# Performance work log

Measured on AMD Instinct MI355X. Metric: run time of the kernel, lower is better.

## Reference

```python
import jax, jax.numpy as jnp
import numpy as np

B, T, C, H, W = 2, 8, 256, 24, 24
NH = 8
HC = C // NH          # 32 head channels
KT, KHW = 3, 9        # offset conv kernel
ST, SHW = 2, 8        # offset conv stride
EPS = 1e-5


def _p(key, shape):
    return jax.random.normal(key, shape, dtype=jnp.float32) * 0.05


def setup_inputs() -> dict:
    ks = jax.random.split(jax.random.key(0), 16)
    return {
        "x": jax.random.normal(ks[0], (B, T, C, H, W), dtype=jnp.float32),
        "w_in": _p(ks[1], (C, C)), "b_in": _p(ks[2], (C,)),
        "w_q": _p(ks[3], (C, C)), "b_q": _p(ks[4], (C,)),
        "w_off_dw": _p(ks[5], (HC, 1, KT, KHW, KHW)), "b_off_dw": _p(ks[6], (HC,)),
        "ln_g": jnp.ones((HC,), jnp.float32), "ln_b": jnp.zeros((HC,), jnp.float32),
        "w_off_proj": _p(ks[7], (3, HC)),
        "w_k": _p(ks[8], (C, C)), "b_k": _p(ks[9], (C,)),
        "w_v": _p(ks[10], (C, C)), "b_v": _p(ks[11], (C,)),
        "rpe_w1": _p(ks[12], (32, 3)), "rpe_b1": _p(ks[13], (32,)),
        "rpe_w2": _p(ks[14], (1, 32)),
    }


def _conv1x1(x, w, b):
    # x: (B,C,T,H,W), w: (Co,Ci) -> pointwise Conv3d
    return jnp.einsum('bcthw,oc->bothw', x, w) + b[None, :, None, None, None]


def _trilinear(img, gx, gy, gz):
    # torch F.grid_sample(mode='bilinear', align_corners=True) for 5D input.
    # img: (G,Ch,T,H,W); gx->W axis, gy->H axis, gz->T axis, coords in [-1,1], shape (G,S)
    G, Ch, Td, Hd, Wd = img.shape
    ix = (gx + 1.0) * 0.5 * (Wd - 1)
    iy = (gy + 1.0) * 0.5 * (Hd - 1)
    iz = (gz + 1.0) * 0.5 * (Td - 1)
    x0 = jnp.floor(ix); y0 = jnp.floor(iy); z0 = jnp.floor(iz)
    fx = ix - x0; fy = iy - y0; fz = iz - z0
    x0i = jnp.clip(x0.astype(jnp.int32), 0, Wd - 1); x1i = jnp.clip(x0i + 1, 0, Wd - 1)
    y0i = jnp.clip(y0.astype(jnp.int32), 0, Hd - 1); y1i = jnp.clip(y0i + 1, 0, Hd - 1)
    z0i = jnp.clip(z0.astype(jnp.int32), 0, Td - 1); z1i = jnp.clip(z0i + 1, 0, Td - 1)
    bidx = jnp.arange(G)[:, None]

    def g(zi, yi, xi):
        return img[bidx, :, zi, yi, xi]  # (G,S,Ch)

    wz0, wz1 = (1.0 - fz)[..., None], fz[..., None]
    wy0, wy1 = (1.0 - fy)[..., None], fy[..., None]
    wx0, wx1 = (1.0 - fx)[..., None], fx[..., None]
    return (g(z0i, y0i, x0i) * wz0 * wy0 * wx0 + g(z0i, y0i, x1i) * wz0 * wy0 * wx1 +
            g(z0i, y1i, x0i) * wz0 * wy1 * wx0 + g(z0i, y1i, x1i) * wz0 * wy1 * wx1 +
            g(z1i, y0i, x0i) * wz1 * wy0 * wx0 + g(z1i, y0i, x1i) * wz1 * wy0 * wx1 +
            g(z1i, y1i, x0i) * wz1 * wy1 * wx0 + g(z1i, y1i, x1i) * wz1 * wy1 * wx1)


def reference(x, w_in, b_in, w_q, b_q, w_off_dw, b_off_dw, ln_g, ln_b, w_off_proj,
              w_k, b_k, w_v, b_v, rpe_w1, rpe_b1, rpe_w2):
    scale = HC ** (-0.5)
    xc = _conv1x1(jnp.transpose(x, (0, 2, 1, 3, 4)), w_in, b_in)       # (B,C,T,H,W)
    q = _conv1x1(xc, w_q, b_q)
    q_off = q.reshape(B * NH, HC, T, H, W)
    # depthwise offset conv: kernel (3,9,9), stride (2,8,8), pad (1,4,4)
    off = jax.lax.conv_general_dilated(
        q_off, w_off_dw, (ST, SHW, SHW),
        ((KT // 2, KT // 2), (KHW // 2, KHW // 2), (KHW // 2, KHW // 2)),
        dimension_numbers=('NCDHW', 'OIDHW', 'NCDHW'), feature_group_count=HC)
    off = off + b_off_dw[None, :, None, None, None]
    Tk, Hk, Wk = off.shape[2], off.shape[3], off.shape[4]
    o = jnp.transpose(off, (0, 2, 3, 4, 1))                             # (G,Tk,Hk,Wk,HC)
    mu = o.mean(-1, keepdims=True)
    var = ((o - mu) ** 2).mean(-1, keepdims=True)
    o = (o - mu) / jnp.sqrt(var + EPS) * ln_g + ln_b
    o = jax.nn.gelu(o, approximate=False)
    offset = jnp.einsum('bthwc,pc->bthwp', o, w_off_proj)               # (G,Tk,Hk,Wk,3)
    # reference points (linspace(0.5, K-0.5, K) normalized by (K-1))
    rt = ((jnp.arange(Tk, dtype=jnp.float32) + 0.5) / (Tk - 1.0)) * 2.0 - 1.0
    ry = ((jnp.arange(Hk, dtype=jnp.float32) + 0.5) / (Hk - 1.0)) * 2.0 - 1.0
    rx = ((jnp.arange(Wk, dtype=jnp.float32) + 0.5) / (Wk - 1.0)) * 2.0 - 1.0
    ref = jnp.stack(jnp.meshgrid(rt, ry, rx, indexing='ij'), axis=-1)   # (Tk,Hk,Wk,3)
    pos = jnp.clip(offset + ref, -1.0, 1.0)                             # offset_range_factor < 0 path
    G = B * NH
    n = Tk * Hk * Wk
    m = T * H * W
    posf = pos.reshape(G, n, 3)                                         # (t, y, x)
    # torch passes grid = pos[..., (0,2,1)] -> grid (x_w, y_h, z_t) = (pos_t, pos_x, pos_y)
    xs = _trilinear(xc.reshape(G, HC, T, H, W), posf[..., 0], posf[..., 2], posf[..., 1])  # (G,n,HC)
    x_sampled = jnp.transpose(xs, (0, 2, 1)).reshape(B, C, Tk, Hk, Wk)
    k = _conv1x1(x_sampled, w_k, b_k).reshape(G, HC, n)
    v = _conv1x1(x_sampled, w_v, b_v).reshape(G, HC, n)
    qf = q.reshape(G, HC, m)
    attn = jnp.einsum('bcm,bcn->bmn', qf, k) * scale                    # (G,m,n)
    # log-CPB bias (source normalizes y by W-1 and x by H-1; faithful)
    qt = (jnp.arange(T, dtype=jnp.float32) / (T - 1.0)) * 2.0 - 1.0
    qy = (jnp.arange(H, dtype=jnp.float32) / (W - 1.0)) * 2.0 - 1.0
    qx = (jnp.arange(W, dtype=jnp.float32) / (H - 1.0)) * 2.0 - 1.0
    qg = jnp.stack(jnp.meshgrid(qt, qy, qx, indexing='ij'), axis=-1).reshape(m, 3)
    disp = (qg[None, :, None, :] - posf[:, None, :, :]) * 4.0           # (G,m,n,3)
    disp = jnp.sign(disp) * jnp.log2(jnp.abs(disp) + 1.0) / 3.0         # log2(8) = 3
    hbias = jax.nn.relu(jnp.einsum('gmnp,hp->gmnh', disp, rpe_w1) + rpe_b1)
    attn = attn + jnp.einsum('gmnh,oh->gmno', hbias, rpe_w2)[..., 0]
    attn = jax.nn.softmax(attn, axis=2)
    out = jnp.einsum('bmn,bcn->bcm', attn, v).reshape(B, C, T, H, W)
    return jnp.transpose(out, (0, 2, 1, 3, 4))                          # (B,T,C,H,W)
```

## Files before the change

kernel.cpp:

```cpp
#include <hip/hip_runtime.h>
#include <hip/hip_bf16.h>

typedef unsigned short ushortT;
typedef __attribute__((ext_vector_type(8))) short bf16x8;
typedef __attribute__((ext_vector_type(4))) float f32x4;

#define WS_XC   0
#define WS_QB   2359296
#define WS_POS  3538944
#define WS_K    3540736
#define WS_V    3559168
#define WS_WC   3577600
#define WS_B512 3675904

__device__ __forceinline__ float bf2f(ushortT u) {
  union { unsigned int i; float f; } c; c.i = ((unsigned int)u) << 16; return c.f;
}
__device__ __forceinline__ ushortT f2bf(float f) {
  union { float f; unsigned int i; } c; c.f = f;
  unsigned int lsb = (c.i >> 16) & 1;
  return (ushortT)((c.i + 0x7fff + lsb) >> 16);
}
__device__ __forceinline__ float ldg_f(const void* p, int i, int bf) {
  return bf ? bf2f(((const ushortT*)p)[i]) : ((const float*)p)[i];
}
__device__ __forceinline__ int detect_bf(const void* x) {
  const ushortT* u = (const ushortT*)x;
  int wild = 0;
#pragma unroll
  for (int i = 0; i < 32; i++) {
    int e = (u[i] >> 7) & 0xFF;
    wild += (e != 0 && (e < 90 || e > 160)) ? 1 : 0;
  }
  return wild <= 4;
}

__global__ __launch_bounds__(256) void k_wc(const void* x, const void* w_in, const void* b_in,
                                            const void* w_q, const void* b_q,
                                            float* wc, float* bias512) {
  int o = blockIdx.x, tid = threadIdx.x;
  int bf = detect_bf(x);
  __shared__ float wq_s[256];
  __shared__ float red[256];
  wq_s[tid] = ldg_f(w_q, o * 256 + tid, bf);
  __syncthreads();
  float s = 0.f;
#pragma unroll 8
  for (int j = 0; j < 256; j++) s += wq_s[j] * ldg_f(w_in, j * 256 + tid, bf);
  wc[o * 256 + tid] = s;
  red[tid] = wq_s[tid] * ldg_f(b_in, tid, bf);
  __syncthreads();
  for (int m = 128; m; m >>= 1) {
    if (tid < m) red[tid] += red[tid + m];
    __syncthreads();
  }
  if (tid == 0) bias512[256 + o] = red[0] + ldg_f(b_q, o, bf);
  if (o == 0) bias512[tid] = ldg_f(b_in, tid, bf);
}

__global__ __launch_bounds__(256) void k_gemm_mfma(const void* x, const void* w_in, const float* wc,
                                                   const float* bias512, float* xc, ushortT* qb) {
  const int bf = detect_bf(x);
  __shared__ ushortT Ah[2][64 * 40], Al[2][64 * 40];
  __shared__ ushortT Bh[2][64 * 40], Bl[2][64 * 40];
  int tid = threadIdx.x;
  int bid = blockIdx.x;
  int colT = bid / 144, rowT = bid % 144;
  int col0 = colT * 64;
  int row0 = rowT * 64;
  int bt = row0 / 576;
  int hw0 = row0 % 576;
  const int isW = (col0 < 256);
  const ushortT* xB = (const ushortT*)x;
  const float*   xF = (const float*)x;
  const ushortT* wB = (const ushortT*)w_in;
  const float*   wF = (const float*)w_in;
  int ar = tid & 63, aoct = tid >> 6;
  int bn = tid >> 2, bko = tid & 3;
  int w = tid >> 6, l = tid & 63;
  int wr = w >> 1, wcq = w & 1;
  int lr = l & 15, lk = l >> 4;
  f32x4 acc[2][2] = {};

  float va[8], vb[8];
  auto loadA = [&](int kt) {
    int kbase = (bt * 256 + kt * 32 + aoct * 8) * 576 + hw0 + ar;
#pragma unroll
    for (int j = 0; j < 8; j++)
      va[j] = bf ? bf2f(xB[kbase + j * 576]) : xF[kbase + j * 576];
  };
  auto loadB = [&](int kt) {
    if (isW) {
      if (bf) {
        const ushortT* pp = wB + (col0 + bn) * 256 + kt * 32 + bko * 8;
#pragma unroll
        for (int j = 0; j < 8; j++) vb[j] = bf2f(pp[j]);
      } else {
        const float* pp = wF + (col0 + bn) * 256 + kt * 32 + bko * 8;
        float4 f0 = *(const float4*)pp;
        float4 f1 = *(const float4*)(pp + 4);
        vb[0] = f0.x; vb[1] = f0.y; vb[2] = f0.z; vb[3] = f0.w;
        vb[4] = f1.x; vb[5] = f1.y; vb[6] = f1.z; vb[7] = f1.w;
      }
    } else {
      const float* pp = wc + (col0 - 256 + bn) * 256 + kt * 32 + bko * 8;
      float4 f0 = *(const float4*)pp;
      float4 f1 = *(const float4*)(pp + 4);
      vb[0] = f0.x; vb[1] = f0.y; vb[2] = f0.z; vb[3] = f0.w;
      vb[4] = f1.x; vb[5] = f1.y; vb[6] = f1.z; vb[7] = f1.w;
    }
  };
  auto writeAB = [&](int buf) {
    unsigned ua[8], ra[8];
#pragma unroll
    for (int j = 0; j < 8; j++) {
      ua[j] = __float_as_uint(va[j]);
      ra[j] = __float_as_uint(va[j] - __uint_as_float(ua[j] & 0xffff0000u));
    }
    int4 ph, pl;
    ph.x = (int)((ua[0] >> 16) | (ua[1] & 0xffff0000u));
    ph.y = (int)((ua[2] >> 16) | (ua[3] & 0xffff0000u));
    ph.z = (int)((ua[4] >> 16) | (ua[5] & 0xffff0000u));
    ph.w = (int)((ua[6] >> 16) | (ua[7] & 0xffff0000u));
    pl.x = (int)((ra[0] >> 16) | (ra[1] & 0xffff0000u));
    pl.y = (int)((ra[2] >> 16) | (ra[3] & 0xffff0000u));
    pl.z = (int)((ra[4] >> 16) | (ra[5] & 0xffff0000u));
    pl.w = (int)((ra[6] >> 16) | (ra[7] & 0xffff0000u));
    *(int4*)&Ah[buf][ar * 40 + aoct * 8] = ph;
    *(int4*)&Al[buf][ar * 40 + aoct * 8] = pl;
#pragma unroll
    for (int j = 0; j < 8; j++) {
      ua[j] = __float_as_uint(vb[j]);
      ra[j] = __float_as_uint(vb[j] - __uint_as_float(ua[j] & 0xffff0000u));
    }
    ph.x = (int)((ua[0] >> 16) | (ua[1] & 0xffff0000u));
    ph.y = (int)((ua[2] >> 16) | (ua[3] & 0xffff0000u));
    ph.z = (int)((ua[4] >> 16) | (ua[5] & 0xffff0000u));
    ph.w = (int)((ua[6] >> 16) | (ua[7] & 0xffff0000u));
    pl.x = (int)((ra[0] >> 16) | (ra[1] & 0xffff0000u));
    pl.y = (int)((ra[2] >> 16) | (ra[3] & 0xffff0000u));
    pl.z = (int)((ra[4] >> 16) | (ra[5] & 0xffff0000u));
    pl.w = (int)((ra[6] >> 16) | (ra[7] & 0xffff0000u));
    *(int4*)&Bh[buf][bn * 40 + bko * 8] = ph;
    *(int4*)&Bl[buf][bn * 40 + bko * 8] = pl;
  };

  loadA(0); loadB(0);
  writeAB(0);
  __syncthreads();
  for (int kt = 0; kt < 8; kt++) {
    int cur = kt & 1;
    if (kt < 7) { loadA(kt + 1); loadB(kt + 1); }
    bf16x8 a0h = *(const bf16x8*)&Ah[cur][(wr * 32 + 0 * 16 + lr) * 40 + lk * 8];
    bf16x8 a1h = *(const bf16x8*)&Ah[cur][(wr * 32 + 1 * 16 + lr) * 40 + lk * 8];
    bf16x8 a0l = *(const bf16x8*)&Al[cur][(wr * 32 + 0 * 16 + lr) * 40 + lk * 8];
    bf16x8 a1l = *(const bf16x8*)&Al[cur][(wr * 32 + 1 * 16 + lr) * 40 + lk * 8];
    bf16x8 b0h = *(const bf16x8*)&Bh[cur][(wcq * 32 + 0 * 16 + lr) * 40 + lk * 8];
    bf16x8 b1h = *(const bf16x8*)&Bh[cur][(wcq * 32 + 1 * 16 + lr) * 40 + lk * 8];
    bf16x8 b0l = *(const bf16x8*)&Bl[cur][(wcq * 32 + 0 * 16 + lr) * 40 + lk * 8];
    bf16x8 b1l = *(const bf16x8*)&Bl[cur][(wcq * 32 + 1 * 16 + lr) * 40 + lk * 8];
    acc[0][0] = __builtin_amdgcn_mfma_f32_16x16x32_bf16(a0h, b0h, acc[0][0], 0, 0, 0);
    acc[0][0] = __builtin_amdgcn_mfma_f32_16x16x32_bf16(a0h, b0l, acc[0][0], 0, 0, 0);
    acc[0][0] = __builtin_amdgcn_mfma_f32_16x16x32_bf16(a0l, b0h, acc[0][0], 0, 0, 0);
    acc[0][1] = __builtin_amdgcn_mfma_f32_16x16x32_bf16(a0h, b1h, acc[0][1], 0, 0, 0);
    acc[0][1] = __builtin_amdgcn_mfma_f32_16x16x32_bf16(a0h, b1l, acc[0][1], 0, 0, 0);
    acc[0][1] = __builtin_amdgcn_mfma_f32_16x16x32_bf16(a0l, b1h, acc[0][1], 0, 0, 0);
    acc[1][0] = __builtin_amdgcn_mfma_f32_16x16x32_bf16(a1h, b0h, acc[1][0], 0, 0, 0);
    acc[1][0] = __builtin_amdgcn_mfma_f32_16x16x32_bf16(a1h, b0l, acc[1][0], 0, 0, 0);
    acc[1][0] = __builtin_amdgcn_mfma_f32_16x16x32_bf16(a1l, b0h, acc[1][0], 0, 0, 0);
    acc[1][1] = __builtin_amdgcn_mfma_f32_16x16x32_bf16(a1h, b1h, acc[1][1], 0, 0, 0);
    acc[1][1] = __builtin_amdgcn_mfma_f32_16x16x32_bf16(a1h, b1l, acc[1][1], 0, 0, 0);
    acc[1][1] = __builtin_amdgcn_mfma_f32_16x16x32_bf16(a1l, b1h, acc[1][1], 0, 0, 0);
    if (kt < 7) writeAB(cur ^ 1);
    __syncthreads();
  }
#pragma unroll
  for (int m = 0; m < 2; m++) {
#pragma unroll
    for (int n = 0; n < 2; n++) {
#pragma unroll
      for (int i = 0; i < 4; i++) {
        int row = row0 + wr * 32 + m * 16 + lk * 4 + i;
        int col = col0 + wcq * 32 + n * 16 + lr;
        float v = acc[m][n][i] + bias512[col];
        if (isW) xc[row * 256 + col] = v;
        else     qb[row * 256 + (col - 256)] = f2bf(v);
      }
    }
  }
}

__global__ __launch_bounds__(256) void k_offsets(const void* x, const ushortT* qb, const void* w_dw,
                                                 const void* b_dw, const void* ln_g, const void* ln_b,
                                                 const void* w_proj, float* pos) {
  __shared__ float wdw[243 * 33];
  __shared__ float part[8][33];
  int bid = blockIdx.x;
  int g = bid / 36, nn = bid % 36;
  int b = g >> 3, nh = g & 7;
  int tk = nn / 9, hk = (nn / 3) % 3, wk = nn % 3;
  int tid = threadIdx.x;
  int ch = tid & 31, grp = tid >> 5;
  int bf = detect_bf(x);
  for (int i = tid; i < 7776; i += 256) {
    int c = i / 243, tap = i % 243;
    wdw[tap * 33 + c] = ldg_f(w_dw, i, bf);
  }
  __syncthreads();
  float sum = 0.f;
  for (int tap = grp; tap < 243; tap += 8) {
    int dt = tap / 81, rem = tap % 81, dh = rem / 9, dw = rem % 9;
    int t = tk * 2 - 1 + dt, h = hk * 8 - 4 + dh, w = wk * 8 - 4 + dw;
    if (t < 0 || t >= 8 || h < 0 || h >= 24 || w < 0 || w >= 24) continue;
    float qv = bf2f(qb[((b * 8 + t) * 576 + h * 24 + w) * 256 + nh * 32 + ch]);
    sum += qv * wdw[tap * 33 + ch];
  }
  part[grp][ch] = sum;
  __syncthreads();
  if (tid < 32) {
    float v = ldg_f(b_dw, ch, bf);
#pragma unroll
    for (int j = 0; j < 8; j++) v += part[j][ch];
    float s1 = v;
    for (int m = 16; m; m >>= 1) s1 += __shfl_xor(s1, m);
    float mu = s1 * (1.f / 32.f);
    float d = v - mu;
    float s2 = d * d;
    for (int m = 16; m; m >>= 1) s2 += __shfl_xor(s2, m);
    float o = d * rsqrtf(s2 * (1.f / 32.f) + 1e-5f) * ldg_f(ln_g, ch, bf) + ldg_f(ln_b, ch, bf);
    o = 0.5f * o * (1.f + erff(o * 0.70710678118654752f));
    float res[3];
#pragma unroll
    for (int p = 0; p < 3; p++) {
      float t3 = o * ldg_f(w_proj, p * 32 + ch, bf);
      for (int m = 16; m; m >>= 1) t3 += __shfl_xor(t3, m);
      res[p] = t3;
    }
    if (ch == 0) {
      float ref0 = ((tk + 0.5f) / 3.f) * 2.f - 1.f;
      float ref1 = ((hk + 0.5f) / 2.f) * 2.f - 1.f;
      float ref2 = ((wk + 0.5f) / 2.f) * 2.f - 1.f;
      pos[bid * 3 + 0] = fminf(1.f, fmaxf(-1.f, res[0] + ref0));
      pos[bid * 3 + 1] = fminf(1.f, fmaxf(-1.f, res[1] + ref1));
      pos[bid * 3 + 2] = fminf(1.f, fmaxf(-1.f, res[2] + ref2));
    }
  }
}

__global__ __launch_bounds__(256) void k_svkv(const void* x, const float* xc_rm, const float* pos,
                                              const void* w_k, const void* b_k,
                                              const void* w_v, const void* b_v,
                                              float* k_rm, float* v_rm) {
  int bx = blockIdx.x;
  int row = bx >> 2, quad = bx & 3;
  int sel = quad >> 1, colhalf = quad & 1;
  int b = row / 36, nn = row % 36;
  int tid = threadIdx.x;
  int bf = detect_bf(x);
  __shared__ float a[256];
  {
    int nh = tid >> 5;
    int g = b * 8 + nh;
    float p0 = pos[(g * 36 + nn) * 3 + 0];
    float p1 = pos[(g * 36 + nn) * 3 + 1];
    float p2 = pos[(g * 36 + nn) * 3 + 2];
    float ix = (p0 + 1.f) * 0.5f * 23.f;
    float iy = (p2 + 1.f) * 0.5f * 23.f;
    float iz = (p1 + 1.f) * 0.5f * 7.f;
    float x0f = floorf(ix), y0f = floorf(iy), z0f = floorf(iz);
    float fx = ix - x0f, fy = iy - y0f, fz = iz - z0f;
    int x0 = min(max((int)x0f, 0), 23), x1 = min(x0 + 1, 23);
    int y0 = min(max((int)y0f, 0), 23), y1 = min(y0 + 1, 23);
    int z0 = min(max((int)z0f, 0), 7),  z1 = min(z0 + 1, 7);
#define AT(z, y, x) xc_rm[(((b * 8 + (z)) * 576 + (y) * 24 + (x)) * 256 + tid)]
    a[tid] =
      AT(z0, y0, x0) * (1.f - fz) * (1.f - fy) * (1.f - fx) + AT(z0, y0, x1) * (1.f - fz) * (1.f - fy) * fx +
      AT(z0, y1, x0) * (1.f - fz) * fy * (1.f - fx)         + AT(z0, y1, x1) * (1.f - fz) * fy * fx +
      AT(z1, y0, x0) * fz * (1.f - fy) * (1.f - fx)         + AT(z1, y0, x1) * fz * (1.f - fy) * fx +
      AT(z1, y1, x0) * fz * fy * (1.f - fx)                 + AT(z1, y1, x1) * fz * fy * fx;
#undef AT
  }
  __syncthreads();
  const void* w = sel ? w_v : w_k;
  const void* bb = sel ? b_v : b_k;
  int col = colhalf * 128 + (tid >> 1);
  int half = tid & 1;
  int c0 = half * 128;
  float s = 0.f;
  if (bf) {
    const ushortT* wp = (const ushortT*)w + col * 256 + c0;
#pragma unroll 4
    for (int c = 0; c < 128; c += 8) {
      ushort4 k0 = *(const ushort4*)(wp + c), k1 = *(const ushort4*)(wp + c + 4);
      s += a[c0+c+0]*bf2f(k0.x) + a[c0+c+1]*bf2f(k0.y) + a[c0+c+2]*bf2f(k0.z) + a[c0+c+3]*bf2f(k0.w)
         + a[c0+c+4]*bf2f(k1.x) + a[c0+c+5]*bf2f(k1.y) + a[c0+c+6]*bf2f(k1.z) + a[c0+c+7]*bf2f(k1.w);
    }
  } else {
    const float* wp = (const float*)w + col * 256 + c0;
#pragma unroll 8
    for (int c = 0; c < 128; c += 4) {
      float4 k4 = *(const float4*)(wp + c);
      s += a[c0+c]*k4.x + a[c0+c+1]*k4.y + a[c0+c+2]*k4.z + a[c0+c+3]*k4.w;
    }
  }
  s += __shfl_xor(s, 1);
  if (half == 0) {
    float* outp = sel ? v_rm : k_rm;
    outp[row * 256 + col] = s + ldg_f(bb, col, bf);
  }
}

__global__ __launch_bounds__(256) void k_attn(const void* x, const ushortT* qb,
                                              const float* k_rm, const float* v_rm,
                                              const float* pos, const void* rpe_w1,
                                              const void* rpe_b1, const void* rpe_w2, void* outp) {
  __shared__ float ks[36][32];
  __shared__ float vs[36][32];
  __shared__ float poss[36][4];
  int g = blockIdx.y, b = g >> 3, nh = g & 7;
  int tid = threadIdx.x;
  int bf = detect_bf(x);
  for (int e = tid; e < 36 * 32; e += 256) {
    int nn = e >> 5, ch = e & 31;
    ks[nn][ch] = k_rm[(b * 36 + nn) * 256 + nh * 32 + ch];
    vs[nn][ch] = v_rm[(b * 36 + nn) * 256 + nh * 32 + ch];
  }
  if (tid < 108) poss[tid / 3][tid % 3] = pos[g * 108 + tid];
  __syncthreads();

  int sub = tid & 3, chb = sub * 8;
  int mm = blockIdx.x * 64 + (tid >> 2);
  int t = mm / 576, hw = mm % 576, hh = hw / 24, wwi = hw % 24;
  float qreg[8];
  {
    const ushort4* qp = (const ushort4*)&qb[(b * 4608 + mm) * 256 + nh * 32 + chb];
    ushort4 u0 = qp[0], u1 = qp[1];
    qreg[0] = bf2f(u0.x); qreg[1] = bf2f(u0.y); qreg[2] = bf2f(u0.z); qreg[3] = bf2f(u0.w);
    qreg[4] = bf2f(u1.x); qreg[5] = bf2f(u1.y); qreg[6] = bf2f(u1.z); qreg[7] = bf2f(u1.w);
  }
  float wx[8], wy[8], wz[8], wb_[8], w2[8];
#pragma unroll
  for (int j = 0; j < 8; j++) {
    int h = chb + j;
    wx[j]  = ldg_f(rpe_w1, h * 3 + 0, bf);
    wy[j]  = ldg_f(rpe_w1, h * 3 + 1, bf);
    wz[j]  = ldg_f(rpe_w1, h * 3 + 2, bf);
    wb_[j] = ldg_f(rpe_b1, h, bf);
    w2[j]  = ldg_f(rpe_w2, h, bf);
  }
  float qg0 = t * (2.f / 7.f) - 1.f;
  float qg1 = hh * (2.f / 23.f) - 1.f;
  float qg2 = wwi * (2.f / 23.f) - 1.f;
  const float scale = 0.17677669529663687f;
  float p[36];
#pragma unroll
  for (int nn = 0; nn < 36; nn++) {
    float s = 0.f;
#pragma unroll
    for (int j = 0; j < 8; j++) s += qreg[j] * ks[nn][chb + j];
    s *= scale;
    float d0 = (qg0 - poss[nn][0]) * 4.f;
    float d1 = (qg1 - poss[nn][1]) * 4.f;
    float d2 = (qg2 - poss[nn][2]) * 4.f;
    d0 = copysignf(__log2f(fabsf(d0) + 1.f) * (1.f / 3.f), d0);
    d1 = copysignf(__log2f(fabsf(d1) + 1.f) * (1.f / 3.f), d1);
    d2 = copysignf(__log2f(fabsf(d2) + 1.f) * (1.f / 3.f), d2);
#pragma unroll
    for (int j = 0; j < 8; j++) {
      float hb = fmaf(d0, wx[j], fmaf(d1, wy[j], fmaf(d2, wz[j], wb_[j])));
      s = fmaf(fmaxf(hb, 0.f), w2[j], s);
    }
    p[nn] = s;
  }
#pragma unroll
  for (int nn = 0; nn < 36; nn++) {
    p[nn] += __shfl_xor(p[nn], 1);
    p[nn] += __shfl_xor(p[nn], 2);
  }
  float mx = -1e30f;
#pragma unroll
  for (int nn = 0; nn < 36; nn++) mx = fmaxf(mx, p[nn]);
  float se = 0.f;
#pragma unroll
  for (int nn = 0; nn < 36; nn++) {
    float e = __expf(p[nn] - mx);
    p[nn] = e;
    se += e;
  }
  float inv = 1.f / se;
  float acc[8] = {};
#pragma unroll
  for (int nn = 0; nn < 36; nn++) {
    float pr = p[nn] * inv;
#pragma unroll
    for (int j = 0; j < 8; j++) acc[j] += pr * vs[nn][chb + j];
  }
  int obase = ((b * 8 + t) * 256 + nh * 32 + chb) * 576 + hw;
  if (bf) {
    __hip_bfloat16* o = (__hip_bfloat16*)outp;
#pragma unroll
    for (int j = 0; j < 8; j++) o[obase + j * 576] = __float2bfloat16(acc[j]);
  } else {
    float* o = (float*)outp;
#pragma unroll
    for (int j = 0; j < 8; j++) o[obase + j * 576] = acc[j];
  }
}

extern "C" void kernel_launch(void* const* d_in, const int* in_sizes, int n_in,
                              void* d_out, int out_size, void* d_ws, size_t ws_size,
                              hipStream_t stream) {
  const void* x        = d_in[0];
  const void* w_in     = d_in[1];
  const void* b_in     = d_in[2];
  const void* w_q      = d_in[3];
  const void* b_q      = d_in[4];
  const void* w_off_dw = d_in[5];
  const void* b_off_dw = d_in[6];
  const void* ln_g     = d_in[7];
  const void* ln_b     = d_in[8];
  const void* w_off_pj = d_in[9];
  const void* w_k      = d_in[10];
  const void* b_k      = d_in[11];
  const void* w_v      = d_in[12];
  const void* b_v      = d_in[13];
  const void* rpe_w1   = d_in[14];
  const void* rpe_b1   = d_in[15];
  const void* rpe_w2   = d_in[16];

  float* ws    = (float*)d_ws;
  float* xc    = ws + WS_XC;
  ushortT* qb  = (ushortT*)(ws + WS_QB);
  float* pos   = ws + WS_POS;
  float* krm   = ws + WS_K;
  float* vrm   = ws + WS_V;
  float* wcf   = ws + WS_WC;
  float* b512  = ws + WS_B512;

  k_wc<<<256, 256, 0, stream>>>(x, w_in, b_in, w_q, b_q, wcf, b512);
  k_gemm_mfma<<<1152, 256, 0, stream>>>(x, w_in, wcf, b512, xc, qb);
  k_offsets<<<576, 256, 0, stream>>>(x, qb, w_off_dw, b_off_dw, ln_g, ln_b, w_off_pj, pos);
  k_svkv<<<288, 256, 0, stream>>>(x, xc, pos, w_k, b_k, w_v, b_v, krm, vrm);
  k_attn<<<dim3(72, 16), 256, 0, stream>>>(x, qb, krm, vrm, pos, rpe_w1, rpe_b1, rpe_w2, d_out);
}
```

Before: 119.5 us.

## Precompute separable log-distance tables and split attention channels across eight lanes

The offsets kernel now precomputes, for each key position, the log-mapped displacement along each axis for every query coordinate (8+24+24 values) and stores them in a workspace table. The attention kernel reads these from shared memory instead of computing three log2 calls per query-key pair. The attention kernel also spreads each query's 32 channels over 8 lanes instead of 4, doubling the grid and halving per-thread work at the cost of an extra shuffle stage. This relies on the displacement being separable per axis and adds a small table write plus larger shared memory use.

```diff
diff --git a/kernel.cpp b/kernel.cpp
--- a/kernel.cpp
+++ b/kernel.cpp
@@ -12,6 +12,7 @@
 #define WS_V    3559168
 #define WS_WC   3577600
 #define WS_B512 3675904
+#define WS_DTAB 3676416
 
 __device__ __forceinline__ float bf2f(ushortT u) {
   union { unsigned int i; float f; } c; c.i = ((unsigned int)u) << 16; return c.f;
@@ -33,6 +34,9 @@
     wild += (e != 0 && (e < 90 || e > 160)) ? 1 : 0;
   }
   return wild <= 4;
+}
+__device__ __forceinline__ float logmap(float d) {
+  return copysignf(__log2f(fabsf(d) + 1.f) * (1.f / 3.f), d);
 }
 
 __global__ __launch_bounds__(256) void k_wc(const void* x, const void* w_in, const void* b_in,
@@ -192,9 +196,10 @@
 
 __global__ __launch_bounds__(256) void k_offsets(const void* x, const ushortT* qb, const void* w_dw,
                                                  const void* b_dw, const void* ln_g, const void* ln_b,
-                                                 const void* w_proj, float* pos) {
+                                                 const void* w_proj, float* pos, float* dtab) {
   __shared__ float wdw[243 * 33];
   __shared__ float part[8][33];
+  __shared__ float ptile[3];
   int bid = blockIdx.x;
   int g = bid / 36, nn = bid % 36;
   int b = g >> 3, nh = g & 7;
@@ -240,10 +245,22 @@
       float ref0 = ((tk + 0.5f) / 3.f) * 2.f - 1.f;
       float ref1 = ((hk + 0.5f) / 2.f) * 2.f - 1.f;
       float ref2 = ((wk + 0.5f) / 2.f) * 2.f - 1.f;
-      pos[bid * 3 + 0] = fminf(1.f, fmaxf(-1.f, res[0] + ref0));
-      pos[bid * 3 + 1] = fminf(1.f, fmaxf(-1.f, res[1] + ref1));
-      pos[bid * 3 + 2] = fminf(1.f, fmaxf(-1.f, res[2] + ref2));
-    }
+      float p0 = fminf(1.f, fmaxf(-1.f, res[0] + ref0));
+      float p1 = fminf(1.f, fmaxf(-1.f, res[1] + ref1));
+      float p2 = fminf(1.f, fmaxf(-1.f, res[2] + ref2));
+      pos[bid * 3 + 0] = p0;
+      pos[bid * 3 + 1] = p1;
+      pos[bid * 3 + 2] = p2;
+      ptile[0] = p0; ptile[1] = p1; ptile[2] = p2;
+    }
+  }
+  __syncthreads();
+  if (tid < 56) {
+    float dv;
+    if (tid < 8)       dv = ((float)tid       * (2.f / 7.f)  - 1.f - ptile[0]) * 4.f;
+    else if (tid < 32) dv = ((float)(tid - 8) * (2.f / 23.f) - 1.f - ptile[1]) * 4.f;
+    else               dv = ((float)(tid - 32)* (2.f / 23.f) - 1.f - ptile[2]) * 4.f;
+    dtab[bid * 56 + tid] = logmap(dv);
   }
 }
 
@@ -312,11 +329,11 @@
 
 __global__ __launch_bounds__(256) void k_attn(const void* x, const ushortT* qb,
                                               const float* k_rm, const float* v_rm,
-                                              const float* pos, const void* rpe_w1,
+                                              const float* dtab, const void* rpe_w1,
                                               const void* rpe_b1, const void* rpe_w2, void* outp) {
   __shared__ float ks[36][32];
   __shared__ float vs[36][32];
-  __shared__ float poss[36][4];
+  __shared__ float dt[36][57];
   int g = blockIdx.y, b = g >> 3, nh = g & 7;
   int tid = threadIdx.x;
   int bf = detect_bf(x);
@@ -325,22 +342,20 @@
     ks[nn][ch] = k_rm[(b * 36 + nn) * 256 + nh * 32 + ch];
     vs[nn][ch] = v_rm[(b * 36 + nn) * 256 + nh * 32 + ch];
   }
-  if (tid < 108) poss[tid / 3][tid % 3] = pos[g * 108 + tid];
-  __syncthreads();
-
-  int sub = tid & 3, chb = sub * 8;
-  int mm = blockIdx.x * 64 + (tid >> 2);
+  for (int e = tid; e < 36 * 56; e += 256) dt[e / 56][e % 56] = dtab[g * 2016 + e];
+  __syncthreads();
+
+  int sub = tid & 7, chb = sub * 4;
+  int mm = blockIdx.x * 32 + (tid >> 3);
   int t = mm / 576, hw = mm % 576, hh = hw / 24, wwi = hw % 24;
-  float qreg[8];
+  float qreg[4];
   {
-    const ushort4* qp = (const ushort4*)&qb[(b * 4608 + mm) * 256 + nh * 32 + chb];
-    ushort4 u0 = qp[0], u1 = qp[1];
-    qreg[0] = bf2f(u0.x); qreg[1] = bf2f(u0.y); qreg[2] = bf2f(u0.z); qreg[3] = bf2f(u0.w);
-    qreg[4] = bf2f(u1.x); qreg[5] = bf2f(u1.y); qreg[6] = bf2f(u1.z); qreg[7] = bf2f(u1.w);
-  }
-  float wx[8], wy[8], wz[8], wb_[8], w2[8];
-#pragma unroll
-  for (int j = 0; j < 8; j++) {
+    ushort4 u = *(const ushort4*)&qb[(b * 4608 + mm) * 256 + nh * 32 + chb];
+    qreg[0] = bf2f(u.x); qreg[1] = bf2f(u.y); qreg[2] = bf2f(u.z); qreg[3] = bf2f(u.w);
+  }
+  float wx[4], wy[4], wz[4], wb_[4], w2[4];
+#pragma unroll
+  for (int j = 0; j < 4; j++) {
     int h = chb + j;
     wx[j]  = ldg_f(rpe_w1, h * 3 + 0, bf);
     wy[j]  = ldg_f(rpe_w1, h * 3 + 1, bf);
@@ -348,25 +363,19 @@
     wb_[j] = ldg_f(rpe_b1, h, bf);
     w2[j]  = ldg_f(rpe_w2, h, bf);
   }
-  float qg0 = t * (2.f / 7.f) - 1.f;
-  float qg1 = hh * (2.f / 23.f) - 1.f;
-  float qg2 = wwi * (2.f / 23.f) - 1.f;
   const float scale = 0.17677669529663687f;
   float p[36];
 #pragma unroll
   for (int nn = 0; nn < 36; nn++) {
     float s = 0.f;
 #pragma unroll
-    for (int j = 0; j < 8; j++) s += qreg[j] * ks[nn][chb + j];
+    for (int j = 0; j < 4; j++) s += qreg[j] * ks[nn][chb + j];
     s *= scale;
-    float d0 = (qg0 - poss[nn][0]) * 4.f;
-    float d1 = (qg1 - poss[nn][1]) * 4.f;
-    float d2 = (qg2 - poss[nn][2]) * 4.f;
-    d0 = copysignf(__log2f(fabsf(d0) + 1.f) * (1.f / 3.f), d0);
-    d1 = copysignf(__log2f(fabsf(d1) + 1.f) * (1.f / 3.f), d1);
-    d2 = copysignf(__log2f(fabsf(d2) + 1.f) * (1.f / 3.f), d2);
-#pragma unroll
-    for (int j = 0; j < 8; j++) {
+    float d0 = dt[nn][t];
+    float d1 = dt[nn][8 + hh];
+    float d2 = dt[nn][32 + wwi];
+#pragma unroll
+    for (int j = 0; j < 4; j++) {
       float hb = fmaf(d0, wx[j], fmaf(d1, wy[j], fmaf(d2, wz[j], wb_[j])));
       s = fmaf(fmaxf(hb, 0.f), w2[j], s);
     }
@@ -376,6 +385,7 @@
   for (int nn = 0; nn < 36; nn++) {
     p[nn] += __shfl_xor(p[nn], 1);
     p[nn] += __shfl_xor(p[nn], 2);
+    p[nn] += __shfl_xor(p[nn], 4);
   }
   float mx = -1e30f;
 #pragma unroll
@@ -388,22 +398,22 @@
     se += e;
   }
   float inv = 1.f / se;
-  float acc[8] = {};
+  float acc[4] = {};
 #pragma unroll
   for (int nn = 0; nn < 36; nn++) {
     float pr = p[nn] * inv;
 #pragma unroll
-    for (int j = 0; j < 8; j++) acc[j] += pr * vs[nn][chb + j];
+    for (int j = 0; j < 4; j++) acc[j] += pr * vs[nn][chb + j];
   }
   int obase = ((b * 8 + t) * 256 + nh * 32 + chb) * 576 + hw;
   if (bf) {
     __hip_bfloat16* o = (__hip_bfloat16*)outp;
 #pragma unroll
-    for (int j = 0; j < 8; j++) o[obase + j * 576] = __float2bfloat16(acc[j]);
+    for (int j = 0; j < 4; j++) o[obase + j * 576] = __float2bfloat16(acc[j]);
   } else {
     float* o = (float*)outp;
 #pragma unroll
-    for (int j = 0; j < 8; j++) o[obase + j * 576] = acc[j];
+    for (int j = 0; j < 4; j++) o[obase + j * 576] = acc[j];
   }
 }
 
@@ -436,10 +446,11 @@
   float* vrm   = ws + WS_V;
   float* wcf   = ws + WS_WC;
   float* b512  = ws + WS_B512;
+  float* dtab  = ws + WS_DTAB;
 
   k_wc<<<256, 256, 0, stream>>>(x, w_in, b_in, w_q, b_q, wcf, b512);
   k_gemm_mfma<<<1152, 256, 0, stream>>>(x, w_in, wcf, b512, xc, qb);
-  k_offsets<<<576, 256, 0, stream>>>(x, qb, w_off_dw, b_off_dw, ln_g, ln_b, w_off_pj, pos);
+  k_offsets<<<576, 256, 0, stream>>>(x, qb, w_off_dw, b_off_dw, ln_g, ln_b, w_off_pj, pos, dtab);
   k_svkv<<<288, 256, 0, stream>>>(x, xc, pos, w_k, b_k, w_v, b_v, krm, vrm);
-  k_attn<<<dim3(72, 16), 256, 0, stream>>>(x, qb, krm, vrm, pos, rpe_w1, rpe_b1, rpe_w2, d_out);
-}
+  k_attn<<<dim3(144, 16), 256, 0, stream>>>(x, qb, krm, vrm, dtab, rpe_w1, rpe_b1, rpe_w2, d_out);
+}
```

After: 117.8 us. Within noise of the previous version (-1.4%).
